# Optimization experiments

Measured on AMD Instinct MI355X. Metric: run time of the kernel, lower is better.

The kernel has to match this reference:

```python
import jax, jax.numpy as jnp
import numpy as np
import itertools

NBX = NBY = 6
NUM_BLOCKS = NBX * NBY

def _build_adj():
    adj = []
    for i, j in itertools.product(range(NBX), range(NBY)):
        for dx, dy in [(-1, 0), (0, -1), (0, 1), (1, 0)]:
            x, y = i + dx, j + dy
            if 0 <= x < NBX and 0 <= y < NBY:
                adj.append((j * NBX + i, y * NBX + x))
    return np.array(adj, dtype=np.int32)

ADJ = _build_adj()                                   # [E=120, 2] (src, dst)
NUM_EDGES = ADJ.shape[0]
# composition structure: edge e' can be extended by edge e iff dst(e') == src(e)
COMP = (ADJ[:, 1][:, None] == ADJ[:, 0][None, :]).astype(np.float32)  # [E, E]
MAX_PATH_LEN = NUM_BLOCKS                            # 36 fixed-point iterations


def setup_inputs() -> dict:
    key = jax.random.key(0)
    ks = jax.random.split(key, 10)
    w = lambda k, shape: jax.random.normal(k, shape, jnp.float32) * 0.05
    d = {}
    d["image"] = jax.random.normal(ks[0], (1024, 1, 32, 32), jnp.float32)
    d["conv1_w"] = w(ks[1], (32, 1, 5, 5));   d["conv1_b"] = jnp.zeros((32,), jnp.float32)
    d["conv2_w"] = w(ks[2], (32, 32, 5, 5));  d["conv2_b"] = jnp.zeros((32,), jnp.float32)
    d["conv3_w"] = w(ks[3], (64, 32, 5, 5));  d["conv3_b"] = jnp.zeros((64,), jnp.float32)
    d["conv4_w"] = w(ks[4], (64, 64, 5, 5));  d["conv4_b"] = jnp.zeros((64,), jnp.float32)
    d["ep_w1"] = w(ks[5], (256, 256));        d["ep_b1"] = jnp.zeros((256,), jnp.float32)
    d["ep_w2"] = w(ks[6], (NUM_BLOCKS, 256)); d["ep_b2"] = jnp.zeros((NUM_BLOCKS,), jnp.float32)
    d["conn_w1"] = w(ks[7], (256, 256));      d["conn_b1"] = jnp.zeros((256,), jnp.float32)
    d["conn_w2"] = w(ks[8], (NUM_EDGES, 256)); d["conn_b2"] = jnp.zeros((NUM_EDGES,), jnp.float32)
    return d


def _conv(x, w, b):
    y = jax.lax.conv_general_dilated(x, w, (1, 1), 'VALID',
                                     dimension_numbers=('NCHW', 'OIHW', 'NCHW'))
    return y + b[None, :, None, None]


def _pool2(x):
    return jax.lax.reduce_window(x, -jnp.inf, jax.lax.max,
                                 (1, 1, 2, 2), (1, 1, 2, 2), 'VALID')


def reference(image, conv1_w, conv1_b, conv2_w, conv2_b, conv3_w, conv3_b,
              conv4_w, conv4_b, ep_w1, ep_b1, ep_w2, ep_b2,
              conn_w1, conn_b1, conn_w2, conn_b2):
    # --- CNN feature extractor (NCHW, torch-flatten order) ---
    x = _conv(image, conv1_w, conv1_b)      # [B,32,28,28]
    x = _conv(x, conv2_w, conv2_b)          # [B,32,24,24]
    x = _pool2(x)                           # [B,32,12,12]
    x = _conv(x, conv3_w, conv3_b)          # [B,64,8,8]
    x = _conv(x, conv4_w, conv4_b)          # [B,64,4,4]
    x = _pool2(x)                           # [B,64,2,2]
    emb = x.reshape(x.shape[0], -1)         # [B,256]

    # --- heads ---
    conn = jax.nn.sigmoid(jax.nn.relu(emb @ conn_w1.T + conn_b1) @ conn_w2.T + conn_b2)  # [B,E]
    ep = jax.nn.sigmoid(jax.nn.relu(emb @ ep_w1.T + ep_b1) @ ep_w2.T + ep_b2)            # [B,36]

    # --- recursive path building under DAMP semiring (add=clipped sum, mult=product) ---
    comp = jnp.asarray(COMP)                # [E,E]: dst(e')==src(e)
    def step(carry, _):
        old, recent = carry
        # extend_path/extend_path_cond: new symbol is the edge itself, prob = (sum_paths_ending_at_src) * p_edge
        new = jnp.clip(recent @ comp, 0.0, 1.0) * conn   # [B,E]
        merged = jnp.clip(old + new, 0.0, 1.0)           # merge (|) with DAMP add
        return (merged, new), None
    (merged, _), _ = jax.lax.scan(step, (conn, conn), None, length=MAX_PATH_LEN)

    # is_endpoint: apply_if with first_index_check / last_index_check (semiring mult)
    src = jnp.asarray(ADJ[:, 0])
    dst = jnp.asarray(ADJ[:, 1])
    paths = merged * ep[:, src] * ep[:, dst]             # [B,E]
    return paths[:, 0]
```

## Files before the change

### kernel.cpp

```cpp
#include <hip/hip_runtime.h>
#include <math.h>

typedef __attribute__((ext_vector_type(8))) short short8;
typedef __attribute__((ext_vector_type(4))) float float4v;
typedef __attribute__((ext_vector_type(4))) unsigned short ushort4v;

static __device__ __forceinline__ unsigned short f2bf(float f) {
    union { float f; unsigned u; } v; v.f = f;
    unsigned u = v.u;
    return (unsigned short)((u + 0x7fffu + ((u >> 16) & 1u)) >> 16);
}
static __device__ __forceinline__ float bf2f(unsigned short h) {
    union { unsigned u; float f; } v; v.u = ((unsigned)h) << 16;
    return v.f;
}
static __device__ __forceinline__ unsigned pk2(float a, float b) {
    return (unsigned)f2bf(a) | ((unsigned)f2bf(b) << 16);
}

struct AdjT {
    int src[120];
    int dst[120];
    int cnt[36];
    int idx[36][4];
    int ostart[36];
    int ocnt[36];
};

constexpr AdjT build_adj() {
    AdjT a{};
    const int ddx[4] = {-1, 0, 0, 1};
    const int ddy[4] = {0, -1, 1, 0};
    int ne = 0;
    for (int i = 0; i < 6; i++)
        for (int j = 0; j < 6; j++)
            for (int d = 0; d < 4; d++) {
                int x = i + ddx[d], y = j + ddy[d];
                if (x >= 0 && x < 6 && y >= 0 && y < 6) {
                    a.src[ne] = j * 6 + i;
                    a.dst[ne] = y * 6 + x;
                    ne++;
                }
            }
    for (int n = 0; n < 36; n++) {
        a.cnt[n] = 0;
        for (int e = 0; e < 120; e++)
            if (a.dst[e] == n) a.idx[n][a.cnt[n]++] = e;
    }
    for (int n = 0; n < 36; n++) { a.ostart[n] = 0; a.ocnt[n] = 0; }
    for (int e = 0; e < 120; e++) {
        a.ocnt[a.src[e]]++;
        if (e == 0 || a.src[e] != a.src[e - 1]) a.ostart[a.src[e]] = e;
    }
    return a;
}

__device__ constexpr AdjT ADJC = build_adj();
__device__ constexpr int G16_START[17] =
    {0, 3, 6, 9, 12, 14, 16, 18, 20, 22, 24, 26, 28, 30, 32, 34, 36};

__global__ __launch_bounds__(256) void k_prepall(
    const float* __restrict__ w1, const float* __restrict__ b1,
    const float* __restrict__ w2, const float* __restrict__ b2,
    const float* __restrict__ w3, const float* __restrict__ w4,
    const float* __restrict__ cnw1, const float* __restrict__ epw1,
    const float* __restrict__ cnw2, const float* __restrict__ epw2,
    unsigned short* __restrict__ wpc, float* __restrict__ wcb,
    unsigned short* __restrict__ wp3, unsigned short* __restrict__ wp4,
    unsigned short* __restrict__ wph1, unsigned short* __restrict__ wpcn2,
    unsigned short* __restrict__ wpep2) {
    __shared__ float s_w1[800];
    __shared__ float s_w2[800];
    if (blockIdx.x < 32) {
        const int co = blockIdx.x, tid = threadIdx.x;
        for (int i = tid; i < 800; i += 256) {
            s_w1[i] = w1[i];
            s_w2[i] = w2[co * 800 + i];
        }
        __syncthreads();
        if (tid < 96) {
            int t = tid;
            float val = 0.f;
            if (t < 81) {
                int ty = t / 9, tx = t - 9 * ty;
                int ylo = ty > 4 ? ty - 4 : 0, yhi = ty < 4 ? ty : 4;
                int xlo = tx > 4 ? tx - 4 : 0, xhi = tx < 4 ? tx : 4;
                for (int k1y = ylo; k1y <= yhi; k1y++)
                    for (int k1x = xlo; k1x <= xhi; k1x++) {
                        int o1 = k1y * 5 + k1x;
                        int o2 = (ty - k1y) * 5 + (tx - k1x);
#pragma unroll
                        for (int ci = 0; ci < 32; ci++)
                            val += s_w1[ci * 25 + o1] * s_w2[ci * 25 + o2];
                    }
            }
            int n = co >> 1, nt = co & 1;
            int ks = t >> 5, r = t & 31, q = r >> 3, j = r & 7;
            wpc[ks * 1024 + nt * 512 + (q * 16 + n) * 8 + j] = f2bf(val);
        } else if (tid == 96) {
            float s = b2[co];
            for (int ci = 0; ci < 32; ci++) {
                float ws = 0.f;
#pragma unroll
                for (int t2 = 0; t2 < 25; t2++) ws += s_w2[ci * 25 + t2];
                s += b1[ci] * ws;
            }
            wcb[co] = s;
        }
        return;
    }
    int e = (blockIdx.x - 32) * 256 + threadIdx.x;
    if (e < 51200) {
        int j = e & 7, lane = (e >> 3) & 63, nt = (e >> 9) & 3, t = e >> 11;
        int co = 4 * (lane & 15) + nt, ci = (lane >> 4) * 8 + j;
        wp3[e] = f2bf(w3[(co * 32 + ci) * 25 + t]);
    } else if (e < 153600) {
        int e4 = e - 51200;
        int j = e4 & 7, lane = (e4 >> 3) & 63, nt = (e4 >> 9) & 3;
        int ks = (e4 >> 11) & 1, t = e4 >> 12;
        int co = 4 * (lane & 15) + nt, ci = ks * 32 + (lane >> 4) * 8 + j;
        wp4[e4] = f2bf(w4[(co * 64 + ci) * 25 + t]);
    } else {
        int eh = e - 153600;
        if (eh < 131072) {
            int j = eh & 7, lane = (eh >> 3) & 63, nt = (eh >> 9) & 31, kt = eh >> 14;
            int c = nt * 16 + (lane & 15);
            int k = kt * 32 + ((lane >> 4) << 3) + j;
            float v = (c < 256) ? cnw1[c * 256 + k] : epw1[(c - 256) * 256 + k];
            wph1[eh] = f2bf(v);
        } else if (eh < 163840) {
            int e2 = eh - 131072;
            int j = e2 & 7, lane = (e2 >> 3) & 63, nt = (e2 >> 9) & 7, kt = e2 >> 12;
            int c = nt * 16 + (lane & 15);
            int k = kt * 32 + ((lane >> 4) << 3) + j;
            wpcn2[e2] = f2bf(c < 120 ? cnw2[c * 256 + k] : 0.f);
        } else {
            int e3 = eh - 163840;
            int j = e3 & 7, lane = (e3 >> 3) & 63, idx = e3 >> 9;
            int kt = idx / 3, nt = idx - kt * 3;
            int c = nt * 16 + (lane & 15);
            int k = kt * 32 + ((lane >> 4) << 3) + j;
            wpep2[e3] = f2bf(c < 36 ? epw2[c * 256 + k] : 0.f);
        }
    }
}

__global__ __launch_bounds__(512) void k_convall(
    const float* __restrict__ img,
    const unsigned short* __restrict__ wpc, const float* __restrict__ wcb,
    const unsigned short* __restrict__ wp3, const float* __restrict__ b3,
    const unsigned short* __restrict__ wp4, const float* __restrict__ b4,
    unsigned short* __restrict__ emb) {
    __shared__ __align__(16) unsigned short s_imgbf[32 * 36];
    __shared__ __align__(16) unsigned short s_buf[10368];
    const int b = blockIdx.x, tid = threadIdx.x;
    const int lane = tid & 63, wave = tid >> 6;
    const int m = lane & 15, quad = lane >> 4;
    const int C3O = 5760;

    if (tid < 256) {
        float4 t = ((const float4*)(img + (size_t)b * 1024))[tid];
        ushort4v pkv;
        pkv[0] = f2bf(t.x); pkv[1] = f2bf(t.y);
        pkv[2] = f2bf(t.z); pkv[3] = f2bf(t.w);
        *(ushort4v*)(s_imgbf + (tid >> 3) * 36 + (tid & 7) * 4) = pkv;
    }

    const short8* wqc = (const short8*)wpc;
    short8 cb0[3], cb1[3];
#pragma unroll
    for (int ks = 0; ks < 3; ks++) {
        cb0[ks] = wqc[(ks * 2 + 0) * 64 + lane];
        cb1[ks] = wqc[(ks * 2 + 1) * 64 + lane];
    }
    const float bc0 = wcb[2 * m], bc1 = wcb[2 * m + 1];
    int ct[3][8];
#pragma unroll
    for (int ks = 0; ks < 3; ks++)
#pragma unroll
        for (int j = 0; j < 8; j++) {
            int t = ks * 32 + quad * 8 + j;
            int toff = 0;
            if (t < 81) {
                int ty = (t * 57) >> 9;
                toff = ty * 36 + (t - 9 * ty);
            }
            ct[ks][j] = toff;
        }
    const short8* wq3 = (const short8*)wp3;

    __syncthreads();

    for (int T = wave; T < 36; T += 8) {
        int pg = T * 4 + (m >> 2);
        int py = (pg * 171) >> 11;
        int px = pg - py * 12;
        int wb = (2 * py + ((m & 3) >> 1)) * 36 + 2 * px + (m & 1);
        float4v a0 = {0.f, 0.f, 0.f, 0.f};
        float4v a1 = {0.f, 0.f, 0.f, 0.f};
#pragma unroll
        for (int ks = 0; ks < 3; ks++) {
            short8 av;
#pragma unroll
            for (int j = 0; j < 8; j++) av[j] = (short)s_imgbf[wb + ct[ks][j]];
            a0 = __builtin_amdgcn_mfma_f32_16x16x32_bf16(av, cb0[ks], a0, 0, 0, 0);
            a1 = __builtin_amdgcn_mfma_f32_16x16x32_bf16(av, cb1[ks], a1, 0, 0, 0);
        }
        float mx0 = fmaxf(fmaxf(a0[0], a0[1]), fmaxf(a0[2], a0[3])) + bc0;
        float mx1 = fmaxf(fmaxf(a1[0], a1[1]), fmaxf(a1[2], a1[3])) + bc1;
        int row = T * 4 + quad;
        *(unsigned*)(s_buf + row * 40 + 2 * m) = pk2(mx0, mx1);
    }
    __syncthreads();

    {
        int pos3 = (wave >> 1) * 16 + m;
        int y3 = pos3 >> 3, x3 = pos3 & 7;
        int a3 = (y3 * 12 + x3) * 40 + quad * 8;
        int nt0 = (wave & 1) * 2;
        float4v acc3[2];
        acc3[0] = (float4v){0.f, 0.f, 0.f, 0.f};
        acc3[1] = (float4v){0.f, 0.f, 0.f, 0.f};
        short8 bw3[2];
        bw3[0] = wq3[nt0 * 64 + lane];
        bw3[1] = wq3[(nt0 + 1) * 64 + lane];
        for (int t = 0; t < 25; t++) {
            short8 nb3[2];
            if (t < 24) {
                nb3[0] = wq3[((t + 1) * 4 + nt0) * 64 + lane];
                nb3[1] = wq3[((t + 1) * 4 + nt0 + 1) * 64 + lane];
            }
            const int ky = t / 5, kx = t - ky * 5;
            short8 av = *(const short8*)(s_buf + a3 + (ky * 12 + kx) * 40);
            acc3[0] = __builtin_amdgcn_mfma_f32_16x16x32_bf16(av, bw3[0], acc3[0], 0, 0, 0);
            acc3[1] = __builtin_amdgcn_mfma_f32_16x16x32_bf16(av, bw3[1], acc3[1], 0, 0, 0);
            if (t < 24) { bw3[0] = nb3[0]; bw3[1] = nb3[1]; }
        }
        float bb0 = b3[4 * m + nt0], bb1 = b3[4 * m + nt0 + 1];
#pragma unroll
        for (int r = 0; r < 4; r++) {
            int row3 = (wave >> 1) * 16 + quad * 4 + r;
            *(unsigned*)(s_buf + C3O + row3 * 72 + 4 * m + nt0) =
                pk2(acc3[0][r] + bb0, acc3[1][r] + bb1);
        }
    }
    __syncthreads();

    if (wave < 4) {
        int y4 = m >> 2, x4 = m & 3;
        int a4 = C3O + (y4 * 8 + x4) * 72 + quad * 8;
        float4v acc4 = (float4v){0.f, 0.f, 0.f, 0.f};
        const short8* wq4 = (const short8*)wp4;
        short8 cw0 = wq4[(0 * 4 + wave) * 64 + lane];
        short8 cw1 = wq4[(1 * 4 + wave) * 64 + lane];
        for (int t = 0; t < 25; t++) {
            short8 n0, n1;
            if (t < 24) {
                n0 = wq4[(((t + 1) * 2) * 4 + wave) * 64 + lane];
                n1 = wq4[(((t + 1) * 2 + 1) * 4 + wave) * 64 + lane];
            }
            const int ky = t / 5, kx = t - ky * 5;
            const int toff = (ky * 8 + kx) * 72;
            short8 av0 = *(const short8*)(s_buf + a4 + toff);
            acc4 = __builtin_amdgcn_mfma_f32_16x16x32_bf16(av0, cw0, acc4, 0, 0, 0);
            short8 av1 = *(const short8*)(s_buf + a4 + toff + 32);
            acc4 = __builtin_amdgcn_mfma_f32_16x16x32_bf16(av1, cw1, acc4, 0, 0, 0);
            if (t < 24) { cw0 = n0; cw1 = n1; }
        }
        float* s_c4 = (float*)s_buf;
#pragma unroll
        for (int r = 0; r < 4; r++)
            s_c4[(quad * 4 + r) * 68 + 4 * m + wave] = acc4[r];
    }
    __syncthreads();

    if (tid < 256) {
        const float* s_c4 = (const float*)s_buf;
        int co = tid >> 2, pp = tid & 3;
        int ppy = pp >> 1, ppx = pp & 1;
        float v0 = s_c4[((2 * ppy) * 4 + 2 * ppx) * 68 + co];
        float v1 = s_c4[((2 * ppy) * 4 + 2 * ppx + 1) * 68 + co];
        float v2 = s_c4[((2 * ppy + 1) * 4 + 2 * ppx) * 68 + co];
        float v3 = s_c4[((2 * ppy + 1) * 4 + 2 * ppx + 1) * 68 + co];
        emb[(size_t)b * 256 + tid] =
            f2bf(fmaxf(fmaxf(v0, v1), fmaxf(v2, v3)) + b4[co]);
    }
}

__global__ __launch_bounds__(256) void k_heads(
    const unsigned short* __restrict__ emb,
    const unsigned short* __restrict__ wph1,
    const float* __restrict__ cn_b1, const float* __restrict__ ep_b1,
    const unsigned short* __restrict__ wpcn2, const float* __restrict__ cn_b2,
    const unsigned short* __restrict__ wpep2, const float* __restrict__ ep_b2,
    float* __restrict__ out) {
    __shared__ unsigned short s_hid[16 * 520];
    __shared__ float s_conn[120 * 17];
    __shared__ float s_rec0[120 * 17];
    __shared__ float s_rec1[120 * 17];
    __shared__ float s_ep[36 * 17];
    const int tid = threadIdx.x;
    const int lane = tid & 63, wave = tid >> 6;
    const int m = lane & 15, q = lane >> 4;
    const int b0 = blockIdx.x * 16;

    float4v acc[8];
#pragma unroll
    for (int i = 0; i < 8; i++) acc[i] = (float4v){0.f, 0.f, 0.f, 0.f};
    const short8* wp1 = (const short8*)wph1;
    for (int kt = 0; kt < 8; kt++) {
        short8 av = *(const short8*)(emb + (size_t)(b0 + m) * 256 + kt * 32 + q * 8);
#pragma unroll
        for (int ntl = 0; ntl < 8; ntl++) {
            int nt = wave * 8 + ntl;
            short8 bv = wp1[(kt * 32 + nt) * 64 + lane];
            acc[ntl] = __builtin_amdgcn_mfma_f32_16x16x32_bf16(av, bv, acc[ntl], 0, 0, 0);
        }
    }
#pragma unroll
    for (int ntl = 0; ntl < 8; ntl++) {
        int c = (wave * 8 + ntl) * 16 + m;
        float bb = (c < 256) ? cn_b1[c] : ep_b1[c - 256];
#pragma unroll
        for (int r = 0; r < 4; r++)
            s_hid[(q * 4 + r) * 520 + c] = f2bf(fmaxf(acc[ntl][r] + bb, 0.f));
    }
    __syncthreads();

    for (int job = wave; job < 11; job += 4) {
        const bool isconn = job < 8;
        const int koff = isconn ? 0 : 256;
        float4v a2 = (float4v){0.f, 0.f, 0.f, 0.f};
        for (int kt = 0; kt < 8; kt++) {
            short8 av = *(const short8*)(s_hid + m * 520 + koff + kt * 32 + q * 8);
            short8 bv = isconn
                ? ((const short8*)wpcn2)[(kt * 8 + job) * 64 + lane]
                : ((const short8*)wpep2)[(kt * 3 + (job - 8)) * 64 + lane];
            a2 = __builtin_amdgcn_mfma_f32_16x16x32_bf16(av, bv, a2, 0, 0, 0);
        }
        int c = (isconn ? job : (job - 8)) * 16 + m;
        float bb = isconn ? (c < 120 ? cn_b2[c] : 0.f) : (c < 36 ? ep_b2[c] : 0.f);
#pragma unroll
        for (int r = 0; r < 4; r++) {
            float v = 1.f / (1.f + __expf(-(a2[r] + bb)));
            int row = q * 4 + r;
            if (isconn) {
                if (c < 120) { s_conn[c * 17 + row] = v; s_rec0[c * 17 + row] = v; }
            } else {
                if (c < 36) s_ep[c * 17 + row] = v;
            }
        }
    }
    __syncthreads();

    const int row = tid >> 4, g = tid & 15;
    const int ns = G16_START[g];
    const int nodecnt = G16_START[g + 1] - ns;
    int ie[3][4], icnt[3], os[3], oc[3];
    float cr[3][4];
#pragma unroll
    for (int s = 0; s < 3; s++) {
        if (s < nodecnt) {
            int n = ns + s;
            icnt[s] = ADJC.cnt[n];
#pragma unroll
            for (int qx = 0; qx < 4; qx++) ie[s][qx] = ADJC.idx[n][qx];
            os[s] = ADJC.ostart[n];
            oc[s] = ADJC.ocnt[n];
#pragma unroll
            for (int oe = 0; oe < 4; oe++)
                cr[s][oe] = (oe < oc[s]) ? s_conn[(os[s] + oe) * 17 + row] : 0.f;
        } else {
            icnt[s] = 0; oc[s] = 0; os[s] = 0;
#pragma unroll
            for (int qx = 0; qx < 4; qx++) ie[s][qx] = 0;
#pragma unroll
            for (int oe = 0; oe < 4; oe++) cr[s][oe] = 0.f;
        }
    }
    float old0 = (g == 0) ? s_conn[0 * 17 + row] : 0.f;

    for (int it = 0; it < 36; it++) {
        const float* cur = (it & 1) ? s_rec1 : s_rec0;
        float* nxt = (it & 1) ? s_rec0 : s_rec1;
#pragma unroll
        for (int s = 0; s < 3; s++) {
            float sum = 0.f;
#pragma unroll
            for (int qx = 0; qx < 4; qx++)
                sum += (qx < icnt[s]) ? cur[ie[s][qx] * 17 + row] : 0.f;
            sum = fminf(sum, 1.f);
#pragma unroll
            for (int oe = 0; oe < 4; oe++) {
                if (oe < oc[s]) {
                    int e = os[s] + oe;
                    float nv = sum * cr[s][oe];
                    nxt[e * 17 + row] = nv;
                    if (g == 0 && s == 0 && oe == 0)
                        old0 = fminf(old0 + nv, 1.f);
                }
            }
        }
        __asm__ volatile("s_waitcnt lgkmcnt(0)" ::: "memory");
    }

    if (g == 0)
        out[b0 + row] = old0 * s_ep[0 * 17 + row] * s_ep[6 * 17 + row];
}

extern "C" void kernel_launch(void* const* d_in, const int* in_sizes, int n_in,
                              void* d_out, int out_size, void* d_ws, size_t ws_size,
                              hipStream_t stream) {
    const float* image = (const float*)d_in[0];
    const float* c1w = (const float*)d_in[1];
    const float* c1b = (const float*)d_in[2];
    const float* c2w = (const float*)d_in[3];
    const float* c2b = (const float*)d_in[4];
    const float* c3w = (const float*)d_in[5];
    const float* c3b = (const float*)d_in[6];
    const float* c4w = (const float*)d_in[7];
    const float* c4b = (const float*)d_in[8];
    const float* epw1 = (const float*)d_in[9];
    const float* epb1 = (const float*)d_in[10];
    const float* epw2 = (const float*)d_in[11];
    const float* epb2 = (const float*)d_in[12];
    const float* cnw1 = (const float*)d_in[13];
    const float* cnb1 = (const float*)d_in[14];
    const float* cnw2 = (const float*)d_in[15];
    const float* cnb2 = (const float*)d_in[16];

    const int B = in_sizes[0] / (32 * 32);

    unsigned short* ws = (unsigned short*)d_ws;
    unsigned short* embo = ws;
    unsigned short* wp3 = embo + (size_t)B * 256;
    unsigned short* wp4 = wp3 + 51200;
    unsigned short* wph1 = wp4 + 102400;
    unsigned short* wpcn2 = wph1 + 131072;
    unsigned short* wpep2 = wpcn2 + 32768;
    unsigned short* wpc = wpep2 + 12288;
    float* wcb = (float*)(wpc + 3072);

    k_prepall<<<1320, 256, 0, stream>>>(c1w, c1b, c2w, c2b, c3w, c4w,
                                        cnw1, epw1, cnw2, epw2,
                                        wpc, wcb, wp3, wp4, wph1, wpcn2, wpep2);
    k_convall<<<B, 512, 0, stream>>>(image, wpc, wcb, wp3, c3b, wp4, c4b, embo);
    k_heads<<<B / 16, 256, 0, stream>>>(embo, wph1, cnb1, epb1,
                                        wpcn2, cnb2, wpep2, epb2, (float*)d_out);
}
```

Measured before the change: 167.5 us.

## Process two images per conv block to reuse conv3 weights and fill idle waves

The fused conv kernel now handles two images per 512-thread block, halving the grid. In the conv3 stage each wave covers two M tiles of one image, so each weight fragment loaded from global memory feeds four MFMAs instead of two. In the conv4 stage all eight waves are busy (four per image) instead of only four. The cost is doubled shared memory per block, which may reduce how many blocks fit per CU, and more registers for the extra accumulators.

```diff
diff --git a/kernel.cpp b/kernel.cpp
--- a/kernel.cpp
+++ b/kernel.cpp
@@ -151,19 +151,20 @@
     const unsigned short* __restrict__ wp3, const float* __restrict__ b3,
     const unsigned short* __restrict__ wp4, const float* __restrict__ b4,
     unsigned short* __restrict__ emb) {
-    __shared__ __align__(16) unsigned short s_imgbf[32 * 36];
-    __shared__ __align__(16) unsigned short s_buf[10368];
-    const int b = blockIdx.x, tid = threadIdx.x;
+    __shared__ __align__(16) unsigned short s_imgbf[2 * 32 * 36];
+    __shared__ __align__(16) unsigned short s_buf[2 * 10368];
+    const int b2 = blockIdx.x, tid = threadIdx.x;
     const int lane = tid & 63, wave = tid >> 6;
     const int m = lane & 15, quad = lane >> 4;
     const int C3O = 5760;
 
-    if (tid < 256) {
-        float4 t = ((const float4*)(img + (size_t)b * 1024))[tid];
+    {
+        int simg = tid >> 8, t = tid & 255;
+        float4 v = ((const float4*)(img + (size_t)(2 * b2 + simg) * 1024))[t];
         ushort4v pkv;
-        pkv[0] = f2bf(t.x); pkv[1] = f2bf(t.y);
-        pkv[2] = f2bf(t.z); pkv[3] = f2bf(t.w);
-        *(ushort4v*)(s_imgbf + (tid >> 3) * 36 + (tid & 7) * 4) = pkv;
+        pkv[0] = f2bf(v.x); pkv[1] = f2bf(v.y);
+        pkv[2] = f2bf(v.z); pkv[3] = f2bf(v.w);
+        *(ushort4v*)(s_imgbf + simg * 1152 + (t >> 3) * 36 + (t & 7) * 4) = pkv;
     }
 
     const short8* wqc = (const short8*)wpc;
@@ -191,11 +192,13 @@
 
     __syncthreads();
 
-    for (int T = wave; T < 36; T += 8) {
+    for (int TT = wave; TT < 72; TT += 8) {
+        int ci = TT >= 36 ? 1 : 0;
+        int T = TT - 36 * ci;
         int pg = T * 4 + (m >> 2);
         int py = (pg * 171) >> 11;
         int px = pg - py * 12;
-        int wb = (2 * py + ((m & 3) >> 1)) * 36 + 2 * px + (m & 1);
+        int wb = ci * 1152 + (2 * py + ((m & 3) >> 1)) * 36 + 2 * px + (m & 1);
         float4v a0 = {0.f, 0.f, 0.f, 0.f};
         float4v a1 = {0.f, 0.f, 0.f, 0.f};
 #pragma unroll
@@ -209,18 +212,28 @@
         float mx0 = fmaxf(fmaxf(a0[0], a0[1]), fmaxf(a0[2], a0[3])) + bc0;
         float mx1 = fmaxf(fmaxf(a1[0], a1[1]), fmaxf(a1[2], a1[3])) + bc1;
         int row = T * 4 + quad;
-        *(unsigned*)(s_buf + row * 40 + 2 * m) = pk2(mx0, mx1);
+        *(unsigned*)(s_buf + ci * 10368 + row * 40 + 2 * m) = pk2(mx0, mx1);
     }
     __syncthreads();
 
     {
-        int pos3 = (wave >> 1) * 16 + m;
-        int y3 = pos3 >> 3, x3 = pos3 & 7;
-        int a3 = (y3 * 12 + x3) * 40 + quad * 8;
-        int nt0 = (wave & 1) * 2;
-        float4v acc3[2];
-        acc3[0] = (float4v){0.f, 0.f, 0.f, 0.f};
-        acc3[1] = (float4v){0.f, 0.f, 0.f, 0.f};
+        const int img3 = wave >> 2;
+        const int mt0 = ((wave >> 1) & 1) * 2;
+        const int nt0 = (wave & 1) * 2;
+        const unsigned short* sb = s_buf + img3 * 10368;
+        int a3[2];
+#pragma unroll
+        for (int mi = 0; mi < 2; mi++) {
+            int pos3 = (mt0 + mi) * 16 + m;
+            int y3 = pos3 >> 3, x3 = pos3 & 7;
+            a3[mi] = (y3 * 12 + x3) * 40 + quad * 8;
+        }
+        float4v acc3[2][2];
+#pragma unroll
+        for (int mi = 0; mi < 2; mi++)
+#pragma unroll
+            for (int ni = 0; ni < 2; ni++)
+                acc3[mi][ni] = (float4v){0.f, 0.f, 0.f, 0.f};
         short8 bw3[2];
         bw3[0] = wq3[nt0 * 64 + lane];
         bw3[1] = wq3[(nt0 + 1) * 64 + lane];
@@ -231,58 +244,67 @@
                 nb3[1] = wq3[((t + 1) * 4 + nt0 + 1) * 64 + lane];
             }
             const int ky = t / 5, kx = t - ky * 5;
-            short8 av = *(const short8*)(s_buf + a3 + (ky * 12 + kx) * 40);
-            acc3[0] = __builtin_amdgcn_mfma_f32_16x16x32_bf16(av, bw3[0], acc3[0], 0, 0, 0);
-            acc3[1] = __builtin_amdgcn_mfma_f32_16x16x32_bf16(av, bw3[1], acc3[1], 0, 0, 0);
+            const int toff = (ky * 12 + kx) * 40;
+            short8 av0 = *(const short8*)(sb + a3[0] + toff);
+            short8 av1 = *(const short8*)(sb + a3[1] + toff);
+            acc3[0][0] = __builtin_amdgcn_mfma_f32_16x16x32_bf16(av0, bw3[0], acc3[0][0], 0, 0, 0);
+            acc3[0][1] = __builtin_amdgcn_mfma_f32_16x16x32_bf16(av0, bw3[1], acc3[0][1], 0, 0, 0);
+            acc3[1][0] = __builtin_amdgcn_mfma_f32_16x16x32_bf16(av1, bw3[0], acc3[1][0], 0, 0, 0);
+            acc3[1][1] = __builtin_amdgcn_mfma_f32_16x16x32_bf16(av1, bw3[1], acc3[1][1], 0, 0, 0);
             if (t < 24) { bw3[0] = nb3[0]; bw3[1] = nb3[1]; }
         }
         float bb0 = b3[4 * m + nt0], bb1 = b3[4 * m + nt0 + 1];
 #pragma unroll
-        for (int r = 0; r < 4; r++) {
-            int row3 = (wave >> 1) * 16 + quad * 4 + r;
-            *(unsigned*)(s_buf + C3O + row3 * 72 + 4 * m + nt0) =
-                pk2(acc3[0][r] + bb0, acc3[1][r] + bb1);
-        }
-    }
-    __syncthreads();
-
-    if (wave < 4) {
+        for (int mi = 0; mi < 2; mi++)
+#pragma unroll
+            for (int r = 0; r < 4; r++) {
+                int row3 = (mt0 + mi) * 16 + quad * 4 + r;
+                *(unsigned*)(s_buf + img3 * 10368 + C3O + row3 * 72 + 4 * m + nt0) =
+                    pk2(acc3[mi][0][r] + bb0, acc3[mi][1][r] + bb1);
+            }
+    }
+    __syncthreads();
+
+    {
+        const int img4 = wave >> 2, nt4 = wave & 3;
         int y4 = m >> 2, x4 = m & 3;
+        const unsigned short* sb = s_buf + img4 * 10368;
         int a4 = C3O + (y4 * 8 + x4) * 72 + quad * 8;
         float4v acc4 = (float4v){0.f, 0.f, 0.f, 0.f};
         const short8* wq4 = (const short8*)wp4;
-        short8 cw0 = wq4[(0 * 4 + wave) * 64 + lane];
-        short8 cw1 = wq4[(1 * 4 + wave) * 64 + lane];
+        short8 cw0 = wq4[(0 * 4 + nt4) * 64 + lane];
+        short8 cw1 = wq4[(1 * 4 + nt4) * 64 + lane];
         for (int t = 0; t < 25; t++) {
             short8 n0, n1;
             if (t < 24) {
-                n0 = wq4[(((t + 1) * 2) * 4 + wave) * 64 + lane];
-                n1 = wq4[(((t + 1) * 2 + 1) * 4 + wave) * 64 + lane];
+                n0 = wq4[(((t + 1) * 2) * 4 + nt4) * 64 + lane];
+                n1 = wq4[(((t + 1) * 2 + 1) * 4 + nt4) * 64 + lane];
             }
             const int ky = t / 5, kx = t - ky * 5;
             const int toff = (ky * 8 + kx) * 72;
-            short8 av0 = *(const short8*)(s_buf + a4 + toff);
+            short8 av0 = *(const short8*)(sb + a4 + toff);
             acc4 = __builtin_amdgcn_mfma_f32_16x16x32_bf16(av0, cw0, acc4, 0, 0, 0);
-            short8 av1 = *(const short8*)(s_buf + a4 + toff + 32);
+            short8 av1 = *(const short8*)(sb + a4 + toff + 32);
             acc4 = __builtin_amdgcn_mfma_f32_16x16x32_bf16(av1, cw1, acc4, 0, 0, 0);
             if (t < 24) { cw0 = n0; cw1 = n1; }
         }
-        float* s_c4 = (float*)s_buf;
+        float* s_c4 = (float*)(s_buf + img4 * 10368);
 #pragma unroll
         for (int r = 0; r < 4; r++)
-            s_c4[(quad * 4 + r) * 68 + 4 * m + wave] = acc4[r];
-    }
-    __syncthreads();
-
-    if (tid < 256) {
-        const float* s_c4 = (const float*)s_buf;
-        int co = tid >> 2, pp = tid & 3;
+            s_c4[(quad * 4 + r) * 68 + 4 * m + nt4] = acc4[r];
+    }
+    __syncthreads();
+
+    {
+        const int simg = tid >> 8, t = tid & 255;
+        const float* s_c4 = (const float*)(s_buf + simg * 10368);
+        int co = t >> 2, pp = t & 3;
         int ppy = pp >> 1, ppx = pp & 1;
         float v0 = s_c4[((2 * ppy) * 4 + 2 * ppx) * 68 + co];
         float v1 = s_c4[((2 * ppy) * 4 + 2 * ppx + 1) * 68 + co];
         float v2 = s_c4[((2 * ppy + 1) * 4 + 2 * ppx) * 68 + co];
         float v3 = s_c4[((2 * ppy + 1) * 4 + 2 * ppx + 1) * 68 + co];
-        emb[(size_t)b * 256 + tid] =
+        emb[(size_t)(2 * b2 + simg) * 256 + t] =
             f2bf(fmaxf(fmaxf(v0, v1), fmaxf(v2, v3)) + b4[co]);
     }
 }
@@ -444,7 +466,7 @@
     k_prepall<<<1320, 256, 0, stream>>>(c1w, c1b, c2w, c2b, c3w, c4w,
                                         cnw1, epw1, cnw2, epw2,
                                         wpc, wcb, wp3, wp4, wph1, wpcn2, wpep2);
-    k_convall<<<B, 512, 0, stream>>>(image, wpc, wcb, wp3, c3b, wp4, c4b, embo);
+    k_convall<<<B / 2, 512, 0, stream>>>(image, wpc, wcb, wp3, c3b, wp4, c4b, embo);
     k_heads<<<B / 16, 256, 0, stream>>>(embo, wph1, cnb1, epb1,
                                         wpcn2, cnb2, wpep2, epb2, (float*)d_out);
 }
```

Result: faster. 161.0 us (-3.9%).
